# Kernel optimization log

Measured on AMD Instinct MI355X. Metric: run time of the kernel, lower is better.

The kernel has to match this reference:

```python
import jax, jax.numpy as jnp
import numpy as np

N_NODES = 50000
N_EDGES = 800000


def _gcn_conv(x, W, b, src, dst, n_nodes):
    # GCNConv(normalize=False): out[i] = sum_{(j->i) in E} (x_j @ W) + b
    h = x @ W                                   # [N, d_out]
    agg = jax.ops.segment_sum(h[src], dst, num_segments=n_nodes)  # [N, d_out]
    return agg + b


def setup_inputs() -> dict:
    key = jax.random.key(0)
    ks = jax.random.split(key, 10)
    nfeat, nhid, nclass = 500, 64, 50
    inp = {
        "features": jax.random.normal(ks[0], (N_NODES, nfeat), dtype=jnp.float32),
        "edge_index": jax.random.randint(ks[1], (2, N_EDGES), 0, N_NODES, dtype=jnp.int64),
        "W1": jax.random.normal(ks[2], (nfeat, nhid), dtype=jnp.float32) * (1.0 / np.sqrt(nfeat)),
        "b1": jax.random.normal(ks[3], (nhid,), dtype=jnp.float32) * 0.01,
        "Wc1": jax.random.normal(ks[4], (nhid, nhid), dtype=jnp.float32) * (1.0 / np.sqrt(nhid)),
        "bc1": jax.random.normal(ks[5], (nhid,), dtype=jnp.float32) * 0.01,
        "Wc2": jax.random.normal(ks[6], (2 * nhid, 2 * nhid), dtype=jnp.float32) * (1.0 / np.sqrt(2 * nhid)),
        "bc2": jax.random.normal(ks[7], (2 * nhid,), dtype=jnp.float32) * 0.01,
        "W2": jax.random.normal(ks[8], (7 * nhid, nclass), dtype=jnp.float32) * (1.0 / np.sqrt(7 * nhid)),
        "b2": jax.random.normal(ks[9], (nclass,), dtype=jnp.float32) * 0.01,
    }
    return inp


def reference(features, edge_index, W1, b1, Wc1, bc1, Wc2, bc2, W2, b2):
    n = features.shape[0]
    src, dst = edge_index[0], edge_index[1]  # PyG: messages flow row(src) -> col(dst)

    x = jax.nn.relu(features @ W1 + b1)                       # [N, nhid]
    x11 = _gcn_conv(x, Wc1, bc1, src, dst, n)                 # [N, nhid]
    x12 = _gcn_conv(x11, Wc1, bc1, src, dst, n)               # [N, nhid]
    x1 = jnp.concatenate((x11, x12), axis=-1)                 # [N, 2*nhid]
    x21 = _gcn_conv(x1, Wc2, bc2, src, dst, n)                # [N, 2*nhid]
    x22 = _gcn_conv(x21, Wc2, bc2, src, dst, n)               # [N, 2*nhid]
    x2 = jnp.concatenate((x21, x22), axis=-1)                 # [N, 4*nhid]
    h = jnp.concatenate((x, x1, x2), axis=-1)                 # [N, 7*nhid]
    # dropout omitted (deterministic inference reference)
    return jax.nn.sigmoid(h @ W2 + b2)                        # [N, nclass]
```

## Files before the change

### kernel.cpp

```cpp
#include <hip/hip_runtime.h>
#include <math.h>

#define N_NODES 50000
#define N_EDGES 800000

template<int K, int ACT>
__global__ __launch_bounds__(256) void gemm_rt_kernel(
    const float* __restrict__ A, int lda,
    const float* __restrict__ W, int ldw,
    const float* __restrict__ bias,
    float* __restrict__ out, int ldo, int M)
{
    constexpr int BM = 64, BK = 32;
    constexpr int SAS = 36;
    constexpr int NCH = (K + BK - 1) / BK;
    __shared__ float sA[BM * SAS];
    __shared__ float sW[BK * 64];
    const int tid  = threadIdx.x;
    const int brow = blockIdx.x * BM;
    const int n0   = blockIdx.y * 64;
    const int tn4  = (tid & 15) * 4;
    const int tm4  = (tid >> 4) * 4;

    float acc[4][4];
#pragma unroll
    for (int i = 0; i < 4; ++i)
#pragma unroll
        for (int j = 0; j < 4; ++j) acc[i][j] = 0.f;

    for (int ch = 0; ch < NCH; ++ch) {
        const int k0 = ch * BK;
#pragma unroll
        for (int i = 0; i < 2; ++i) {
            int f = i * 256 + tid;
            int kk = f >> 4, c4 = (f & 15) * 4;
            int gk = k0 + kk;
            float4 v = make_float4(0.f, 0.f, 0.f, 0.f);
            if (gk < K) v = *(const float4*)&W[(size_t)gk * ldw + n0 + c4];
            *(float4*)&sW[kk * 64 + c4] = v;
        }
#pragma unroll
        for (int i = 0; i < 2; ++i) {
            int f = i * 256 + tid;
            int r = f >> 3, c4 = (f & 7) * 4;
            int gr = brow + r, gk = k0 + c4;
            float4 v = make_float4(0.f, 0.f, 0.f, 0.f);
            if (gr < M) {
                if (K % BK == 0 || gk + 3 < K) {
                    v = *(const float4*)&A[(size_t)gr * lda + gk];
                } else {
                    float t0 = (gk + 0 < K) ? A[(size_t)gr * lda + gk + 0] : 0.f;
                    float t1 = (gk + 1 < K) ? A[(size_t)gr * lda + gk + 1] : 0.f;
                    float t2 = (gk + 2 < K) ? A[(size_t)gr * lda + gk + 2] : 0.f;
                    float t3 = (gk + 3 < K) ? A[(size_t)gr * lda + gk + 3] : 0.f;
                    v = make_float4(t0, t1, t2, t3);
                }
            }
            *(float4*)&sA[r * SAS + c4] = v;
        }
        __syncthreads();
#pragma unroll
        for (int kq = 0; kq < BK / 4; ++kq) {
            float a[4][4], w[4][4];
#pragma unroll
            for (int i = 0; i < 4; ++i)
                *(float4*)&a[i][0] = *(const float4*)&sA[(tm4 + i) * SAS + kq * 4];
#pragma unroll
            for (int j = 0; j < 4; ++j)
                *(float4*)&w[j][0] = *(const float4*)&sW[(kq * 4 + j) * 64 + tn4];
#pragma unroll
            for (int i = 0; i < 4; ++i)
#pragma unroll
                for (int k = 0; k < 4; ++k)
#pragma unroll
                    for (int j = 0; j < 4; ++j)
                        acc[i][j] = fmaf(a[i][k], w[k][j], acc[i][j]);
        }
        __syncthreads();
    }

    float4 b = *(const float4*)&bias[n0 + tn4];
#pragma unroll
    for (int i = 0; i < 4; ++i) {
        int gr = brow + tm4 + i;
        if (gr < M) {
            float4 v;
            v.x = acc[i][0] + b.x; v.y = acc[i][1] + b.y;
            v.z = acc[i][2] + b.z; v.w = acc[i][3] + b.w;
            if (ACT == 1) {
                v.x = fmaxf(v.x, 0.f); v.y = fmaxf(v.y, 0.f);
                v.z = fmaxf(v.z, 0.f); v.w = fmaxf(v.w, 0.f);
            }
            *(float4*)&out[(size_t)gr * ldo + n0 + tn4] = v;
        }
    }
}

__global__ __launch_bounds__(256) void zero_kernel(int* __restrict__ p, int n)
{
    int i = blockIdx.x * 256 + threadIdx.x;
    if (i < n) p[i] = 0;
}

__global__ __launch_bounds__(256) void count_kernel(
    const int* __restrict__ dst, int* __restrict__ counts, int ne)
{
    int e = blockIdx.x * 256 + threadIdx.x;
    if (e < ne) atomicAdd(&counts[dst[e]], 1);
}

__global__ __launch_bounds__(256) void scan1_kernel(
    const int* __restrict__ counts, int* __restrict__ local,
    int* __restrict__ bsum, int n)
{
    __shared__ int sd[256];
    const int t = threadIdx.x;
    const int i = blockIdx.x * 256 + t;
    int c = (i < n) ? counts[i] : 0;
    sd[t] = c;
    __syncthreads();
#pragma unroll
    for (int off = 1; off < 256; off <<= 1) {
        int v = (t >= off) ? sd[t - off] : 0;
        __syncthreads();
        sd[t] += v;
        __syncthreads();
    }
    if (i < n) local[i] = sd[t] - c;
    if (t == 255) bsum[blockIdx.x] = sd[255];
}

__global__ __launch_bounds__(256) void scan2_kernel(
    const int* __restrict__ bsum, int* __restrict__ boff, int nb)
{
    __shared__ int sd[256];
    const int t = threadIdx.x;
    int v = (t < nb) ? bsum[t] : 0;
    sd[t] = v;
    __syncthreads();
#pragma unroll
    for (int off = 1; off < 256; off <<= 1) {
        int u = (t >= off) ? sd[t - off] : 0;
        __syncthreads();
        sd[t] += u;
        __syncthreads();
    }
    if (t < nb) boff[t] = sd[t] - v;
}

__global__ __launch_bounds__(256) void scan3_kernel(
    int* __restrict__ row_ptr, const int* __restrict__ boff,
    int* __restrict__ cursor, int n, int total)
{
    const int i = blockIdx.x * 256 + threadIdx.x;
    if (i < n) {
        int v = row_ptr[i] + boff[blockIdx.x];
        row_ptr[i] = v;
        cursor[i]  = v;
    }
    if (i == 0) row_ptr[n] = total;
}

__global__ __launch_bounds__(256) void fill_kernel(
    const int* __restrict__ src, const int* __restrict__ dst,
    int* __restrict__ cursor, int* __restrict__ elist, int ne)
{
    int e = blockIdx.x * 256 + threadIdx.x;
    if (e < ne) {
        int p = atomicAdd(&cursor[dst[e]], 1);
        elist[p] = src[e];
    }
}

template<int D>
__global__ __launch_bounds__(256) void agg_kernel(
    const float* __restrict__ h, int ldh,
    const int* __restrict__ row_ptr, const int* __restrict__ elist,
    float* __restrict__ out, int ldo, int n)
{
    constexpr int LPR = D / 4;
    constexpr int EPI = 64 / LPR;
    const int lane = threadIdx.x & 63;
    const int node = blockIdx.x * 4 + (threadIdx.x >> 6);
    if (node >= n) return;
    const int g  = lane / LPR;
    const int c4 = (lane % LPR) * 4;
    const int beg = row_ptr[node], end = row_ptr[node + 1];

    float4 acc = make_float4(0.f, 0.f, 0.f, 0.f);
    for (int e = beg + g; e < end; e += EPI) {
        int s = elist[e];
        float4 v = *(const float4*)&h[(size_t)s * ldh + c4];
        acc.x += v.x; acc.y += v.y; acc.z += v.z; acc.w += v.w;
    }
    if (EPI == 4) {
        acc.x += __shfl_xor(acc.x, 16); acc.y += __shfl_xor(acc.y, 16);
        acc.z += __shfl_xor(acc.z, 16); acc.w += __shfl_xor(acc.w, 16);
    }
    acc.x += __shfl_xor(acc.x, 32); acc.y += __shfl_xor(acc.y, 32);
    acc.z += __shfl_xor(acc.z, 32); acc.w += __shfl_xor(acc.w, 32);

    if (g == 0)
        *(float4*)&out[(size_t)node * ldo + c4] = acc;
}

__global__ __launch_bounds__(256) void final_kernel(
    const float* __restrict__ X,
    const float* __restrict__ X1,
    const float* __restrict__ X2,
    const float* __restrict__ W2,
    const float* __restrict__ b2,
    float* __restrict__ out, int M)
{
    constexpr int BM = 64, BK = 32, NC = 50, SAS = 36;
    __shared__ float sA[BM * SAS];
    __shared__ float sW[BK * 64];
    const int tid  = threadIdx.x;
    const int brow = blockIdx.x * BM;
    const int tn4  = (tid & 15) * 4;
    const int tm4  = (tid >> 4) * 4;

    float acc[4][4];
#pragma unroll
    for (int i = 0; i < 4; ++i)
#pragma unroll
        for (int j = 0; j < 4; ++j) acc[i][j] = 0.f;

    for (int ch = 0; ch < 14; ++ch) {
        const float* Ap; int lda, off;
        if (ch < 2)      { Ap = X;  lda = 64;  off = ch * 32; }
        else if (ch < 6) { Ap = X1; lda = 128; off = (ch - 2) * 32; }
        else             { Ap = X2; lda = 256; off = (ch - 6) * 32; }

        for (int i = tid; i < BK * 64; i += 256) {
            int kk = i >> 6, c = i & 63;
            int gk = ch * 32 + kk;
            sW[i] = (c < NC) ? W2[gk * NC + c] : 0.f;
        }
#pragma unroll
        for (int i = 0; i < 2; ++i) {
            int f = i * 256 + tid;
            int r = f >> 3, c4 = (f & 7) * 4;
            int gr = brow + r;
            float4 v = make_float4(0.f, 0.f, 0.f, 0.f);
            if (gr < M) v = *(const float4*)&Ap[(size_t)gr * lda + off + c4];
            *(float4*)&sA[r * SAS + c4] = v;
        }
        __syncthreads();
#pragma unroll
        for (int kq = 0; kq < BK / 4; ++kq) {
            float a[4][4], w[4][4];
#pragma unroll
            for (int i = 0; i < 4; ++i)
                *(float4*)&a[i][0] = *(const float4*)&sA[(tm4 + i) * SAS + kq * 4];
#pragma unroll
            for (int j = 0; j < 4; ++j)
                *(float4*)&w[j][0] = *(const float4*)&sW[(kq * 4 + j) * 64 + tn4];
#pragma unroll
            for (int i = 0; i < 4; ++i)
#pragma unroll
                for (int k = 0; k < 4; ++k)
#pragma unroll
                    for (int j = 0; j < 4; ++j)
                        acc[i][j] = fmaf(a[i][k], w[k][j], acc[i][j]);
        }
        __syncthreads();
    }

#pragma unroll
    for (int i = 0; i < 4; ++i) {
        int gr = brow + tm4 + i;
        if (gr < M) {
#pragma unroll
            for (int j = 0; j < 4; ++j) {
                int c = tn4 + j;
                if (c < NC) {
                    float v = acc[i][j] + b2[c];
                    out[(size_t)gr * NC + c] = 1.f / (1.f + expf(-v));
                }
            }
        }
    }
}

extern "C" void kernel_launch(void* const* d_in, const int* in_sizes, int n_in,
                              void* d_out, int out_size, void* d_ws, size_t ws_size,
                              hipStream_t stream)
{
    const float* features = (const float*)d_in[0];
    const int*   ei       = (const int*)d_in[1];
    const float* W1  = (const float*)d_in[2];
    const float* b1  = (const float*)d_in[3];
    const float* Wc1 = (const float*)d_in[4];
    const float* bc1 = (const float*)d_in[5];
    const float* Wc2 = (const float*)d_in[6];
    const float* bc2 = (const float*)d_in[7];
    const float* W2  = (const float*)d_in[8];
    const float* b2  = (const float*)d_in[9];
    float* out = (float*)d_out;

    const int* src = ei;
    const int* dst = ei + N_EDGES;

    float* X  = (float*)d_ws;
    float* X1 = X  + (size_t)N_NODES * 64;
    float* X2 = X1 + (size_t)N_NODES * 128;
    float* G  = X2 + (size_t)N_NODES * 256;
    int* counts  = (int*)(G + (size_t)N_NODES * 128);
    int* cursor  = counts + N_NODES;
    int* row_ptr = cursor + N_NODES;
    int* elist   = row_ptr + (N_NODES + 1);
    int* bsum    = elist + N_EDGES;
    int* boff    = bsum + 256;

    const int MB = (N_NODES + 63) / 64;
    const int EB = (N_EDGES + 255) / 256;
    const int NB = (N_NODES + 255) / 256;
    const int AB = (N_NODES + 3) / 4;

    zero_kernel<<<NB, 256, 0, stream>>>(counts, N_NODES);
    count_kernel<<<EB, 256, 0, stream>>>(dst, counts, N_EDGES);
    scan1_kernel<<<NB, 256, 0, stream>>>(counts, row_ptr, bsum, N_NODES);
    scan2_kernel<<<1, 256, 0, stream>>>(bsum, boff, NB);
    scan3_kernel<<<NB, 256, 0, stream>>>(row_ptr, boff, cursor, N_NODES, N_EDGES);
    fill_kernel<<<EB, 256, 0, stream>>>(src, dst, cursor, elist, N_EDGES);

    gemm_rt_kernel<500, 1><<<dim3(MB, 1), 256, 0, stream>>>(
        features, 500, W1, 64, b1, X, 64, N_NODES);

    agg_kernel<64><<<AB, 256, 0, stream>>>(X, 64, row_ptr, elist, G, 128, N_NODES);
    gemm_rt_kernel<64, 0><<<dim3(MB, 1), 256, 0, stream>>>(
        G, 128, Wc1, 64, bc1, X1, 128, N_NODES);

    agg_kernel<64><<<AB, 256, 0, stream>>>(X1, 128, row_ptr, elist, G, 128, N_NODES);
    gemm_rt_kernel<64, 0><<<dim3(MB, 1), 256, 0, stream>>>(
        G, 128, Wc1, 64, bc1, X1 + 64, 128, N_NODES);

    agg_kernel<64><<<AB, 256, 0, stream>>>(X1 + 64, 128, row_ptr, elist, G + 64, 128, N_NODES);
    gemm_rt_kernel<128, 0><<<dim3(MB, 2), 256, 0, stream>>>(
        G, 128, Wc2, 128, bc2, X2, 256, N_NODES);

    agg_kernel<128><<<AB, 256, 0, stream>>>(X2, 256, row_ptr, elist, G, 128, N_NODES);
    gemm_rt_kernel<128, 0><<<dim3(MB, 2), 256, 0, stream>>>(
        G, 128, Wc2, 128, bc2, X2 + 128, 256, N_NODES);

    final_kernel<<<MB, 256, 0, stream>>>(X, X1, X2, W2, b2, out, N_NODES);
}
```

Measured before the change: 604.6 us.

## Use split-bf16 MFMA GEMMs and store activations as hi/lo bf16 planes

```diff
diff --git a/kernel.cpp b/kernel.cpp
--- a/kernel.cpp
+++ b/kernel.cpp
@@ -4,96 +4,264 @@
 #define N_NODES 50000
 #define N_EDGES 800000
 
+typedef short bf16x8 __attribute__((ext_vector_type(8)));
+typedef float f32x4 __attribute__((ext_vector_type(4)));
+
+__device__ __forceinline__ ushort f2bf(float f) {
+    unsigned u = __float_as_uint(f);
+    u += 0x7fffu + ((u >> 16) & 1u);
+    return (ushort)(u >> 16);
+}
+__device__ __forceinline__ float bf2f(ushort h) {
+    return __uint_as_float(((unsigned)h) << 16);
+}
+__device__ __forceinline__ void split2(float a, ushort& h, ushort& l) {
+    h = f2bf(a);
+    l = f2bf(a - bf2f(h));
+}
+
+__global__ __launch_bounds__(256) void convert_wt_kernel(
+    const float* __restrict__ W, int K, int N, int KP, int NP,
+    ushort* __restrict__ Th, ushort* __restrict__ Tl)
+{
+    int i = blockIdx.x * 256 + threadIdx.x;
+    if (i >= NP * KP) return;
+    int n = i / KP, k = i % KP;
+    float v = (k < K && n < N) ? W[(size_t)k * N + n] : 0.f;
+    ushort h, l;
+    split2(v, h, l);
+    Th[(size_t)n * KP + k] = h;
+    Tl[(size_t)n * KP + k] = l;
+}
+
+__device__ __forceinline__ void stage_B_lds(
+    const ushort* __restrict__ WTh, const ushort* __restrict__ WTl,
+    int n0, int KP, int k0, ushort* sBh, ushort* sBl, int tid)
+{
+    for (int i = tid; i < 512; i += 256) {
+        int pl = i >> 8, s = i & 255, row = s >> 2, q = s & 3;
+        const ushort* src = pl ? WTl : WTh;
+        uint4 v = *(const uint4*)&src[(size_t)(n0 + row) * KP + k0 + q * 8];
+        ushort* d = pl ? sBl : sBh;
+        *(uint4*)&d[row * 40 + q * 8] = v;
+    }
+}
+
+__device__ __forceinline__ void stage_A_planes(
+    const ushort* __restrict__ Ahi, const ushort* __restrict__ Alo,
+    int lda, int brow, int M, int k0, ushort* sAh, ushort* sAl, int tid)
+{
+    for (int i = tid; i < 1024; i += 256) {
+        int pl = i >> 9, s = i & 511, row = s >> 2, q = s & 3;
+        int gr = brow + row;
+        uint4 v = make_uint4(0u, 0u, 0u, 0u);
+        const ushort* src = pl ? Alo : Ahi;
+        if (gr < M) v = *(const uint4*)&src[(size_t)gr * lda + k0 + q * 8];
+        ushort* d = pl ? sAl : sAh;
+        *(uint4*)&d[row * 40 + q * 8] = v;
+    }
+}
+
+__device__ __forceinline__ void mfma_compute(
+    const ushort* sAh, const ushort* sAl,
+    const ushort* sBh, const ushort* sBl,
+    int lane, int wr, int wc, f32x4 acc[4][2])
+{
+    bf16x8 ah[4], al[4], bh[2], bl[2];
+#pragma unroll
+    for (int mi = 0; mi < 4; ++mi) {
+        int off = (wr + mi * 16 + (lane & 15)) * 40 + (lane >> 4) * 8;
+        ah[mi] = *(const bf16x8*)&sAh[off];
+        al[mi] = *(const bf16x8*)&sAl[off];
+    }
+#pragma unroll
+    for (int ni = 0; ni < 2; ++ni) {
+        int off = (wc + ni * 16 + (lane & 15)) * 40 + (lane >> 4) * 8;
+        bh[ni] = *(const bf16x8*)&sBh[off];
+        bl[ni] = *(const bf16x8*)&sBl[off];
+    }
+#pragma unroll
+    for (int mi = 0; mi < 4; ++mi)
+#pragma unroll
+        for (int ni = 0; ni < 2; ++ni) {
+            acc[mi][ni] = __builtin_amdgcn_mfma_f32_16x16x32_bf16(ah[mi], bh[ni], acc[mi][ni], 0, 0, 0);
+            acc[mi][ni] = __builtin_amdgcn_mfma_f32_16x16x32_bf16(ah[mi], bl[ni], acc[mi][ni], 0, 0, 0);
+            acc[mi][ni] = __builtin_amdgcn_mfma_f32_16x16x32_bf16(al[mi], bh[ni], acc[mi][ni], 0, 0, 0);
+        }
+}
+
 template<int K, int ACT>
-__global__ __launch_bounds__(256) void gemm_rt_kernel(
-    const float* __restrict__ A, int lda,
-    const float* __restrict__ W, int ldw,
+__global__ __launch_bounds__(256) void gemm_mfma_kernel(
+    const ushort* __restrict__ Ahi, const ushort* __restrict__ Alo, int lda,
+    const ushort* __restrict__ WTh, const ushort* __restrict__ WTl,
     const float* __restrict__ bias,
-    float* __restrict__ out, int ldo, int M)
-{
-    constexpr int BM = 64, BK = 32;
-    constexpr int SAS = 36;
-    constexpr int NCH = (K + BK - 1) / BK;
-    __shared__ float sA[BM * SAS];
-    __shared__ float sW[BK * 64];
+    ushort* __restrict__ Ohi, ushort* __restrict__ Olo, int ldo, int M)
+{
+    __shared__ ushort sAh[128 * 40], sAl[128 * 40], sBh[64 * 40], sBl[64 * 40];
     const int tid  = threadIdx.x;
-    const int brow = blockIdx.x * BM;
+    const int brow = blockIdx.x * 128;
     const int n0   = blockIdx.y * 64;
-    const int tn4  = (tid & 15) * 4;
-    const int tm4  = (tid >> 4) * 4;
-
-    float acc[4][4];
-#pragma unroll
-    for (int i = 0; i < 4; ++i)
-#pragma unroll
-        for (int j = 0; j < 4; ++j) acc[i][j] = 0.f;
-
-    for (int ch = 0; ch < NCH; ++ch) {
-        const int k0 = ch * BK;
-#pragma unroll
-        for (int i = 0; i < 2; ++i) {
-            int f = i * 256 + tid;
-            int kk = f >> 4, c4 = (f & 15) * 4;
-            int gk = k0 + kk;
-            float4 v = make_float4(0.f, 0.f, 0.f, 0.f);
-            if (gk < K) v = *(const float4*)&W[(size_t)gk * ldw + n0 + c4];
-            *(float4*)&sW[kk * 64 + c4] = v;
+    const int lane = tid & 63, w = tid >> 6;
+    const int wr = (w >> 1) * 64, wc = (w & 1) * 32;
+
+    f32x4 acc[4][2];
+#pragma unroll
+    for (int mi = 0; mi < 4; ++mi)
+#pragma unroll
+        for (int ni = 0; ni < 2; ++ni) acc[mi][ni] = (f32x4)0.f;
+
+    for (int ch = 0; ch < K / 32; ++ch) {
+        const int k0 = ch * 32;
+        stage_A_planes(Ahi, Alo, lda, brow, M, k0, sAh, sAl, tid);
+        stage_B_lds(WTh, WTl, n0, K, k0, sBh, sBl, tid);
+        __syncthreads();
+        mfma_compute(sAh, sAl, sBh, sBl, lane, wr, wc, acc);
+        __syncthreads();
+    }
+
+#pragma unroll
+    for (int mi = 0; mi < 4; ++mi)
+#pragma unroll
+        for (int ni = 0; ni < 2; ++ni) {
+            int col = n0 + wc + ni * 16 + (lane & 15);
+            float b = bias[col];
+#pragma unroll
+            for (int r = 0; r < 4; ++r) {
+                int row = brow + wr + mi * 16 + (lane >> 4) * 4 + r;
+                if (row < M) {
+                    float v = acc[mi][ni][r] + b;
+                    if (ACT == 1) v = fmaxf(v, 0.f);
+                    ushort h, l;
+                    split2(v, h, l);
+                    Ohi[(size_t)row * ldo + col] = h;
+                    Olo[(size_t)row * ldo + col] = l;
+                }
+            }
         }
-#pragma unroll
-        for (int i = 0; i < 2; ++i) {
-            int f = i * 256 + tid;
-            int r = f >> 3, c4 = (f & 7) * 4;
-            int gr = brow + r, gk = k0 + c4;
+}
+
+__global__ __launch_bounds__(256) void gemm_feat_kernel(
+    const float* __restrict__ A,
+    const ushort* __restrict__ WTh, const ushort* __restrict__ WTl,
+    const float* __restrict__ bias,
+    ushort* __restrict__ Ohi, ushort* __restrict__ Olo, int M)
+{
+    __shared__ ushort sAh[128 * 40], sAl[128 * 40], sBh[64 * 40], sBl[64 * 40];
+    const int tid  = threadIdx.x;
+    const int brow = blockIdx.x * 128;
+    const int lane = tid & 63, w = tid >> 6;
+    const int wr = (w >> 1) * 64, wc = (w & 1) * 32;
+
+    f32x4 acc[4][2];
+#pragma unroll
+    for (int mi = 0; mi < 4; ++mi)
+#pragma unroll
+        for (int ni = 0; ni < 2; ++ni) acc[mi][ni] = (f32x4)0.f;
+
+    for (int ch = 0; ch < 16; ++ch) {
+        const int k0 = ch * 32;
+        for (int i = tid; i < 1024; i += 256) {
+            int row = i >> 3, q = i & 7;
+            int gr = brow + row, gk = k0 + q * 4;
             float4 v = make_float4(0.f, 0.f, 0.f, 0.f);
             if (gr < M) {
-                if (K % BK == 0 || gk + 3 < K) {
-                    v = *(const float4*)&A[(size_t)gr * lda + gk];
+                const float* ap = A + (size_t)gr * 500;
+                if (gk + 3 < 500) {
+                    v = *(const float4*)&ap[gk];
                 } else {
-                    float t0 = (gk + 0 < K) ? A[(size_t)gr * lda + gk + 0] : 0.f;
-                    float t1 = (gk + 1 < K) ? A[(size_t)gr * lda + gk + 1] : 0.f;
-                    float t2 = (gk + 2 < K) ? A[(size_t)gr * lda + gk + 2] : 0.f;
-                    float t3 = (gk + 3 < K) ? A[(size_t)gr * lda + gk + 3] : 0.f;
-                    v = make_float4(t0, t1, t2, t3);
+                    if (gk + 0 < 500) v.x = ap[gk + 0];
+                    if (gk + 1 < 500) v.y = ap[gk + 1];
+                    if (gk + 2 < 500) v.z = ap[gk + 2];
+                    if (gk + 3 < 500) v.w = ap[gk + 3];
                 }
             }
-            *(float4*)&sA[r * SAS + c4] = v;
+            ushort h0, h1, h2, h3, l0, l1, l2, l3;
+            split2(v.x, h0, l0); split2(v.y, h1, l1);
+            split2(v.z, h2, l2); split2(v.w, h3, l3);
+            uint2 hv, lv;
+            hv.x = (unsigned)h0 | ((unsigned)h1 << 16);
+            hv.y = (unsigned)h2 | ((unsigned)h3 << 16);
+            lv.x = (unsigned)l0 | ((unsigned)l1 << 16);
+            lv.y = (unsigned)l2 | ((unsigned)l3 << 16);
+            *(uint2*)&sAh[row * 40 + q * 4] = hv;
+            *(uint2*)&sAl[row * 40 + q * 4] = lv;
         }
-        __syncthreads();
-#pragma unroll
-        for (int kq = 0; kq < BK / 4; ++kq) {
-            float a[4][4], w[4][4];
-#pragma unroll
-            for (int i = 0; i < 4; ++i)
-                *(float4*)&a[i][0] = *(const float4*)&sA[(tm4 + i) * SAS + kq * 4];
-#pragma unroll
-            for (int j = 0; j < 4; ++j)
-                *(float4*)&w[j][0] = *(const float4*)&sW[(kq * 4 + j) * 64 + tn4];
-#pragma unroll
-            for (int i = 0; i < 4; ++i)
-#pragma unroll
-                for (int k = 0; k < 4; ++k)
-#pragma unroll
-                    for (int j = 0; j < 4; ++j)
-                        acc[i][j] = fmaf(a[i][k], w[k][j], acc[i][j]);
+        stage_B_lds(WTh, WTl, 0, 512, k0, sBh, sBl, tid);
+        __syncthreads();
+        mfma_compute(sAh, sAl, sBh, sBl, lane, wr, wc, acc);
+        __syncthreads();
+    }
+
+#pragma unroll
+    for (int mi = 0; mi < 4; ++mi)
+#pragma unroll
+        for (int ni = 0; ni < 2; ++ni) {
+            int col = wc + ni * 16 + (lane & 15);
+            float b = bias[col];
+#pragma unroll
+            for (int r = 0; r < 4; ++r) {
+                int row = brow + wr + mi * 16 + (lane >> 4) * 4 + r;
+                if (row < M) {
+                    float v = fmaxf(acc[mi][ni][r] + b, 0.f);
+                    ushort h, l;
+                    split2(v, h, l);
+                    Ohi[(size_t)row * 64 + col] = h;
+                    Olo[(size_t)row * 64 + col] = l;
+                }
+            }
         }
-        __syncthreads();
-    }
-
-    float4 b = *(const float4*)&bias[n0 + tn4];
-#pragma unroll
-    for (int i = 0; i < 4; ++i) {
-        int gr = brow + tm4 + i;
-        if (gr < M) {
-            float4 v;
-            v.x = acc[i][0] + b.x; v.y = acc[i][1] + b.y;
-            v.z = acc[i][2] + b.z; v.w = acc[i][3] + b.w;
-            if (ACT == 1) {
-                v.x = fmaxf(v.x, 0.f); v.y = fmaxf(v.y, 0.f);
-                v.z = fmaxf(v.z, 0.f); v.w = fmaxf(v.w, 0.f);
+}
+
+__global__ __launch_bounds__(256) void final_mfma_kernel(
+    const ushort* __restrict__ Xhi,  const ushort* __restrict__ Xlo,
+    const ushort* __restrict__ X1hi, const ushort* __restrict__ X1lo,
+    const ushort* __restrict__ X2hi, const ushort* __restrict__ X2lo,
+    const ushort* __restrict__ WTh,  const ushort* __restrict__ WTl,
+    const float* __restrict__ b2,
+    float* __restrict__ out, int M)
+{
+    __shared__ ushort sAh[128 * 40], sAl[128 * 40], sBh[64 * 40], sBl[64 * 40];
+    const int tid  = threadIdx.x;
+    const int brow = blockIdx.x * 128;
+    const int lane = tid & 63, w = tid >> 6;
+    const int wr = (w >> 1) * 64, wc = (w & 1) * 32;
+
+    f32x4 acc[4][2];
+#pragma unroll
+    for (int mi = 0; mi < 4; ++mi)
+#pragma unroll
+        for (int ni = 0; ni < 2; ++ni) acc[mi][ni] = (f32x4)0.f;
+
+    for (int ch = 0; ch < 14; ++ch) {
+        const ushort *Ah, *Al;
+        int lda, off;
+        if (ch < 2)      { Ah = Xhi;  Al = Xlo;  lda = 64;  off = ch * 32; }
+        else if (ch < 6) { Ah = X1hi; Al = X1lo; lda = 128; off = (ch - 2) * 32; }
+        else             { Ah = X2hi; Al = X2lo; lda = 256; off = (ch - 6) * 32; }
+        stage_A_planes(Ah + off, Al + off, lda, brow, M, 0, sAh, sAl, tid);
+        stage_B_lds(WTh, WTl, 0, 448, ch * 32, sBh, sBl, tid);
+        __syncthreads();
+        mfma_compute(sAh, sAl, sBh, sBl, lane, wr, wc, acc);
+        __syncthreads();
+    }
+
+#pragma unroll
+    for (int mi = 0; mi < 4; ++mi)
+#pragma unroll
+        for (int ni = 0; ni < 2; ++ni) {
+            int col = wc + ni * 16 + (lane & 15);
+            if (col < 50) {
+                float b = b2[col];
+#pragma unroll
+                for (int r = 0; r < 4; ++r) {
+                    int row = brow + wr + mi * 16 + (lane >> 4) * 4 + r;
+                    if (row < M) {
+                        float v = acc[mi][ni][r] + b;
+                        out[(size_t)row * 50 + col] = 1.f / (1.f + expf(-v));
+                    }
+                }
             }
-            *(float4*)&out[(size_t)gr * ldo + n0 + tn4] = v;
         }
-    }
 }
 
 __global__ __launch_bounds__(256) void zero_kernel(int* __restrict__ p, int n)
@@ -173,10 +341,10 @@
 }
 
 template<int D>
-__global__ __launch_bounds__(256) void agg_kernel(
-    const float* __restrict__ h, int ldh,
+__global__ __launch_bounds__(256) void agg_planes_kernel(
+    const ushort* __restrict__ hhi, const ushort* __restrict__ hlo, int ldh,
     const int* __restrict__ row_ptr, const int* __restrict__ elist,
-    float* __restrict__ out, int ldo, int n)
+    ushort* __restrict__ ohi, ushort* __restrict__ olo, int ldo, int n)
 {
     constexpr int LPR = D / 4;
     constexpr int EPI = 64 / LPR;
@@ -187,99 +355,34 @@
     const int c4 = (lane % LPR) * 4;
     const int beg = row_ptr[node], end = row_ptr[node + 1];
 
-    float4 acc = make_float4(0.f, 0.f, 0.f, 0.f);
+    float a0 = 0.f, a1 = 0.f, a2 = 0.f, a3 = 0.f;
     for (int e = beg + g; e < end; e += EPI) {
         int s = elist[e];
-        float4 v = *(const float4*)&h[(size_t)s * ldh + c4];
-        acc.x += v.x; acc.y += v.y; acc.z += v.z; acc.w += v.w;
+        uint2 hv = *(const uint2*)&hhi[(size_t)s * ldh + c4];
+        uint2 lv = *(const uint2*)&hlo[(size_t)s * ldh + c4];
+        a0 += bf2f((ushort)hv.x) + bf2f((ushort)lv.x);
+        a1 += bf2f((ushort)(hv.x >> 16)) + bf2f((ushort)(lv.x >> 16));
+        a2 += bf2f((ushort)hv.y) + bf2f((ushort)lv.y);
+        a3 += bf2f((ushort)(hv.y >> 16)) + bf2f((ushort)(lv.y >> 16));
     }
     if (EPI == 4) {
-        acc.x += __shfl_xor(acc.x, 16); acc.y += __shfl_xor(acc.y, 16);
-        acc.z += __shfl_xor(acc.z, 16); acc.w += __shfl_xor(acc.w, 16);
-    }
-    acc.x += __shfl_xor(acc.x, 32); acc.y += __shfl_xor(acc.y, 32);
-    acc.z += __shfl_xor(acc.z, 32); acc.w += __shfl_xor(acc.w, 32);
-
-    if (g == 0)
-        *(float4*)&out[(size_t)node * ldo + c4] = acc;
-}
-
-__global__ __launch_bounds__(256) void final_kernel(
-    const float* __restrict__ X,
-    const float* __restrict__ X1,
-    const float* __restrict__ X2,
-    const float* __restrict__ W2,
-    const float* __restrict__ b2,
-    float* __restrict__ out, int M)
-{
-    constexpr int BM = 64, BK = 32, NC = 50, SAS = 36;
-    __shared__ float sA[BM * SAS];
-    __shared__ float sW[BK * 64];
-    const int tid  = threadIdx.x;
-    const int brow = blockIdx.x * BM;
-    const int tn4  = (tid & 15) * 4;
-    const int tm4  = (tid >> 4) * 4;
-
-    float acc[4][4];
-#pragma unroll
-    for (int i = 0; i < 4; ++i)
-#pragma unroll
-        for (int j = 0; j < 4; ++j) acc[i][j] = 0.f;
-
-    for (int ch = 0; ch < 14; ++ch) {
-        const float* Ap; int lda, off;
-        if (ch < 2)      { Ap = X;  lda = 64;  off = ch * 32; }
-        else if (ch < 6) { Ap = X1; lda = 128; off = (ch - 2) * 32; }
-        else             { Ap = X2; lda = 256; off = (ch - 6) * 32; }
-
-        for (int i = tid; i < BK * 64; i += 256) {
-            int kk = i >> 6, c = i & 63;
-            int gk = ch * 32 + kk;
-            sW[i] = (c < NC) ? W2[gk * NC + c] : 0.f;
-        }
-#pragma unroll
-        for (int i = 0; i < 2; ++i) {
-            int f = i * 256 + tid;
-            int r = f >> 3, c4 = (f & 7) * 4;
-            int gr = brow + r;
-            float4 v = make_float4(0.f, 0.f, 0.f, 0.f);
-            if (gr < M) v = *(const float4*)&Ap[(size_t)gr * lda + off + c4];
-            *(float4*)&sA[r * SAS + c4] = v;
-        }
-        __syncthreads();
-#pragma unroll
-        for (int kq = 0; kq < BK / 4; ++kq) {
-            float a[4][4], w[4][4];
-#pragma unroll
-            for (int i = 0; i < 4; ++i)
-                *(float4*)&a[i][0] = *(const float4*)&sA[(tm4 + i) * SAS + kq * 4];
-#pragma unroll
-            for (int j = 0; j < 4; ++j)
-                *(float4*)&w[j][0] = *(const float4*)&sW[(kq * 4 + j) * 64 + tn4];
-#pragma unroll
-            for (int i = 0; i < 4; ++i)
-#pragma unroll
-                for (int k = 0; k < 4; ++k)
-#pragma unroll
-                    for (int j = 0; j < 4; ++j)
-                        acc[i][j] = fmaf(a[i][k], w[k][j], acc[i][j]);
-        }
-        __syncthreads();
-    }
-
-#pragma unroll
-    for (int i = 0; i < 4; ++i) {
-        int gr = brow + tm4 + i;
-        if (gr < M) {
-#pragma unroll
-            for (int j = 0; j < 4; ++j) {
-                int c = tn4 + j;
-                if (c < NC) {
-                    float v = acc[i][j] + b2[c];
-                    out[(size_t)gr * NC + c] = 1.f / (1.f + expf(-v));
-                }
-            }
-        }
+        a0 += __shfl_xor(a0, 16); a1 += __shfl_xor(a1, 16);
+        a2 += __shfl_xor(a2, 16); a3 += __shfl_xor(a3, 16);
+    }
+    a0 += __shfl_xor(a0, 32); a1 += __shfl_xor(a1, 32);
+    a2 += __shfl_xor(a2, 32); a3 += __shfl_xor(a3, 32);
+
+    if (g == 0) {
+        ushort h0, h1, h2, h3, l0, l1, l2, l3;
+        split2(a0, h0, l0); split2(a1, h1, l1);
+        split2(a2, h2, l2); split2(a3, h3, l3);
+        uint2 hv, lv;
+        hv.x = (unsigned)h0 | ((unsigned)h1 << 16);
+        hv.y = (unsigned)h2 | ((unsigned)h3 << 16);
+        lv.x = (unsigned)l0 | ((unsigned)l1 << 16);
+        lv.y = (unsigned)l2 | ((unsigned)l3 << 16);
+        *(uint2*)&ohi[(size_t)node * ldo + c4] = hv;
+        *(uint2*)&olo[(size_t)node * ldo + c4] = lv;
     }
 }
 
@@ -302,18 +405,30 @@
     const int* src = ei;
     const int* dst = ei + N_EDGES;
 
-    float* X  = (float*)d_ws;
-    float* X1 = X  + (size_t)N_NODES * 64;
-    float* X2 = X1 + (size_t)N_NODES * 128;
-    float* G  = X2 + (size_t)N_NODES * 256;
-    int* counts  = (int*)(G + (size_t)N_NODES * 128);
+    ushort* Xhi  = (ushort*)d_ws;
+    ushort* Xlo  = Xhi  + (size_t)N_NODES * 64;
+    ushort* X1hi = Xlo  + (size_t)N_NODES * 64;
+    ushort* X1lo = X1hi + (size_t)N_NODES * 128;
+    ushort* X2hi = X1lo + (size_t)N_NODES * 128;
+    ushort* X2lo = X2hi + (size_t)N_NODES * 256;
+    ushort* Ghi  = X2lo + (size_t)N_NODES * 256;
+    ushort* Glo  = Ghi  + (size_t)N_NODES * 128;
+    ushort* W1Th  = Glo  + (size_t)N_NODES * 128;
+    ushort* W1Tl  = W1Th  + 64 * 512;
+    ushort* Wc1Th = W1Tl  + 64 * 512;
+    ushort* Wc1Tl = Wc1Th + 64 * 64;
+    ushort* Wc2Th = Wc1Tl + 64 * 64;
+    ushort* Wc2Tl = Wc2Th + 128 * 128;
+    ushort* W2Th  = Wc2Tl + 128 * 128;
+    ushort* W2Tl  = W2Th  + 64 * 448;
+    int* counts  = (int*)(W2Tl + 64 * 448);
     int* cursor  = counts + N_NODES;
     int* row_ptr = cursor + N_NODES;
     int* elist   = row_ptr + (N_NODES + 1);
     int* bsum    = elist + N_EDGES;
     int* boff    = bsum + 256;
 
-    const int MB = (N_NODES + 63) / 64;
+    const int MB = (N_NODES + 127) / 128;
     const int EB = (N_EDGES + 255) / 256;
     const int NB = (N_NODES + 255) / 256;
     const int AB = (N_NODES + 3) / 4;
@@ -325,24 +440,30 @@
     scan3_kernel<<<NB, 256, 0, stream>>>(row_ptr, boff, cursor, N_NODES, N_EDGES);
     fill_kernel<<<EB, 256, 0, stream>>>(src, dst, cursor, elist, N_EDGES);
 
-    gemm_rt_kernel<500, 1><<<dim3(MB, 1), 256, 0, stream>>>(
-        features, 500, W1, 64, b1, X, 64, N_NODES);
-
-    agg_kernel<64><<<AB, 256, 0, stream>>>(X, 64, row_ptr, elist, G, 128, N_NODES);
-    gemm_rt_kernel<64, 0><<<dim3(MB, 1), 256, 0, stream>>>(
-        G, 128, Wc1, 64, bc1, X1, 128, N_NODES);
-
-    agg_kernel<64><<<AB, 256, 0, stream>>>(X1, 128, row_ptr, elist, G, 128, N_NODES);
-    gemm_rt_kernel<64, 0><<<dim3(MB, 1), 256, 0, stream>>>(
-        G, 128, Wc1, 64, bc1, X1 + 64, 128, N_NODES);
-
-    agg_kernel<64><<<AB, 256, 0, stream>>>(X1 + 64, 128, row_ptr, elist, G + 64, 128, N_NODES);
-    gemm_rt_kernel<128, 0><<<dim3(MB, 2), 256, 0, stream>>>(
-        G, 128, Wc2, 128, bc2, X2, 256, N_NODES);
-
-    agg_kernel<128><<<AB, 256, 0, stream>>>(X2, 256, row_ptr, elist, G, 128, N_NODES);
-    gemm_rt_kernel<128, 0><<<dim3(MB, 2), 256, 0, stream>>>(
-        G, 128, Wc2, 128, bc2, X2 + 128, 256, N_NODES);
-
-    final_kernel<<<MB, 256, 0, stream>>>(X, X1, X2, W2, b2, out, N_NODES);
-}
+    convert_wt_kernel<<<(64 * 512 + 255) / 256, 256, 0, stream>>>(W1, 500, 64, 512, 64, W1Th, W1Tl);
+    convert_wt_kernel<<<(64 * 64 + 255) / 256, 256, 0, stream>>>(Wc1, 64, 64, 64, 64, Wc1Th, Wc1Tl);
+    convert_wt_kernel<<<(128 * 128 + 255) / 256, 256, 0, stream>>>(Wc2, 128, 128, 128, 128, Wc2Th, Wc2Tl);
+    convert_wt_kernel<<<(64 * 448 + 255) / 256, 256, 0, stream>>>(W2, 448, 50, 448, 64, W2Th, W2Tl);
+
+    gemm_feat_kernel<<<MB, 256, 0, stream>>>(features, W1Th, W1Tl, b1, Xhi, Xlo, N_NODES);
+
+    agg_planes_kernel<64><<<AB, 256, 0, stream>>>(Xhi, Xlo, 64, row_ptr, elist, Ghi, Glo, 128, N_NODES);
+    gemm_mfma_kernel<64, 0><<<dim3(MB, 1), 256, 0, stream>>>(
+        Ghi, Glo, 128, Wc1Th, Wc1Tl, bc1, X1hi, X1lo, 128, N_NODES);
+
+    agg_planes_kernel<64><<<AB, 256, 0, stream>>>(X1hi, X1lo, 128, row_ptr, elist, Ghi, Glo, 128, N_NODES);
+    gemm_mfma_kernel<64, 0><<<dim3(MB, 1), 256, 0, stream>>>(
+        Ghi, Glo, 128, Wc1Th, Wc1Tl, bc1, X1hi + 64, X1lo + 64, 128, N_NODES);
+
+    agg_planes_kernel<64><<<AB, 256, 0, stream>>>(X1hi + 64, X1lo + 64, 128, row_ptr, elist,
+                                                  Ghi + 64, Glo + 64, 128, N_NODES);
+    gemm_mfma_kernel<128, 0><<<dim3(MB, 2), 256, 0, stream>>>(
+        Ghi, Glo, 128, Wc2Th, Wc2Tl, bc2, X2hi, X2lo, 256, N_NODES);
+
+    agg_planes_kernel<128><<<AB, 256, 0, stream>>>(X2hi, X2lo, 256, row_ptr, elist, Ghi, Glo, 128, N_NODES);
+    gemm_mfma_kernel<128, 0><<<dim3(MB, 2), 256, 0, stream>>>(
+        Ghi, Glo, 128, Wc2Th, Wc2Tl, bc2, X2hi + 128, X2lo + 128, 256, N_NODES);
+
+    final_mfma_kernel<<<MB, 256, 0, stream>>>(Xhi, Xlo, X1hi, X1lo, X2hi, X2lo,
+                                              W2Th, W2Tl, b2, out, N_NODES);
+}
```

After: 576.0 us. 1.05x faster.
